# Kernel tuning notes

Measured on AMD Instinct MI355X. Metric: run time of the kernel, lower is better.

## Reference

```python
import jax, jax.numpy as jnp
import numpy as np

TOP_K = 2  # num_experts_per_tok


def setup_inputs() -> dict:
    key = jax.random.key(0)
    k1, k2, k3, k4, k5 = jax.random.split(key, 5)
    B, S, D, F, E = 2, 1024, 1024, 2048, 8
    return {
        "x": jax.random.normal(k1, (B, S, D), dtype=jnp.float32),
        "router_kernel_DE": jax.random.normal(k2, (D, E), dtype=jnp.float32) * 0.02,
        "kernel_gating_EDF": jax.random.normal(k3, (E, D, F), dtype=jnp.float32) * 0.02,
        "kernel_up_EDF": jax.random.normal(k4, (E, D, F), dtype=jnp.float32) * 0.02,
        "kernel_down_EFD": jax.random.normal(k5, (E, F, D), dtype=jnp.float32) * 0.02,
    }


def reference(x, router_kernel_DE, kernel_gating_EDF, kernel_up_EDF, kernel_down_EFD):
    E = router_kernel_DE.shape[-1]
    x = x.astype(jnp.float32)
    # --- Router ---
    logits_BSE = jnp.einsum('BSD,DE->BSE', x, router_kernel_DE)
    probs_BSE = jax.nn.softmax(logits_BSE.astype(jnp.float32), axis=-1)
    weights_BSK, indices_BSK = jax.lax.top_k(probs_BSE, TOP_K)
    norm_weights_BSK = jax.nn.softmax(weights_BSK, axis=-1)
    # scatter top-k weights into dense [B,S,E]
    one_hot_BSKE = jax.nn.one_hot(indices_BSK, num_classes=E, dtype=x.dtype)
    full_weights_BSE = jnp.sum(one_hot_BSKE * norm_weights_BSK[..., None], axis=2)
    # --- Dense-over-all-experts MoE forward ---
    gating_BSEF = jnp.einsum('BSD,EDF->BSEF', x, kernel_gating_EDF)
    act_BSEF = jax.nn.silu(gating_BSEF)
    up_BSEF = jnp.einsum('BSD,EDF->BSEF', x, kernel_up_EDF)
    fuse_BSEF = act_BSEF * up_BSEF
    down_BSED = jnp.einsum('BSEF,EFD->BSED', fuse_BSEF, kernel_down_EFD)
    out_BSD = jnp.einsum('BSED,BSE->BSD', down_BSED, full_weights_BSE)
    return out_BSD.astype(jnp.float32)
```

## Files before the change

kernel.cpp:

```cpp
#include <hip/hip_runtime.h>
#include <hip/hip_bf16.h>
#include <stdint.h>

#define T_TOK 2048
#define DIM 1024
#define FDIM 2048
#define NEXP 8
#define NSLOT 4096
#define MAXTILE 64

typedef short bf16x8 __attribute__((ext_vector_type(8)));
typedef unsigned short u16x8 __attribute__((ext_vector_type(8)));
typedef float f32x4 __attribute__((ext_vector_type(4)));

__device__ __forceinline__ unsigned short f2bf(float f) {
  union { float f; unsigned int u; } v; v.f = f;
  unsigned int r = v.u + 0x7FFFu + ((v.u >> 16) & 1u);
  return (unsigned short)(r >> 16);
}

__device__ __forceinline__ float bf2f(unsigned short x) {
  union { unsigned int u; float f; } v; v.u = ((unsigned int)x) << 16;
  return v.f;
}

__device__ __forceinline__ void gld_lds16(const void* g, void* l) {
  __builtin_amdgcn_global_load_lds(
      (const __attribute__((address_space(1))) unsigned int*)g,
      (__attribute__((address_space(3))) unsigned int*)l, 16, 0, 0);
}

__global__ void router_kernel(const float* __restrict__ x, const float* __restrict__ rk,
                              int* __restrict__ counts, int* __restrict__ tok_e,
                              float* __restrict__ tok_w) {
  int w = threadIdx.x >> 6, lane = threadIdx.x & 63;
  int t = blockIdx.x * 4 + w;
  float acc[NEXP];
#pragma unroll
  for (int e = 0; e < NEXP; ++e) acc[e] = 0.f;
  const float4* xr = (const float4*)(x + (size_t)t * DIM);
#pragma unroll
  for (int i = 0; i < 4; ++i) {
    float4 xv = xr[i * 64 + lane];
    int d0 = (i * 64 + lane) * 4;
#pragma unroll
    for (int j = 0; j < 4; ++j) {
      const float4* rr = (const float4*)(rk + (size_t)(d0 + j) * NEXP);
      float4 r0 = rr[0], r1 = rr[1];
      float xs = (j == 0) ? xv.x : (j == 1) ? xv.y : (j == 2) ? xv.z : xv.w;
      acc[0] += xs * r0.x; acc[1] += xs * r0.y; acc[2] += xs * r0.z; acc[3] += xs * r0.w;
      acc[4] += xs * r1.x; acc[5] += xs * r1.y; acc[6] += xs * r1.z; acc[7] += xs * r1.w;
    }
  }
#pragma unroll
  for (int off = 32; off > 0; off >>= 1) {
#pragma unroll
    for (int e = 0; e < NEXP; ++e) acc[e] += __shfl_xor(acc[e], off, 64);
  }
  if (lane == 0) {
    float m = acc[0];
    for (int e = 1; e < NEXP; ++e) m = fmaxf(m, acc[e]);
    float p[NEXP], s = 0.f;
    for (int e = 0; e < NEXP; ++e) { p[e] = expf(acc[e] - m); s += p[e]; }
    float inv = 1.f / s;
    for (int e = 0; e < NEXP; ++e) p[e] *= inv;
    int i1 = 0;
    for (int e = 1; e < NEXP; ++e) if (p[e] > p[i1]) i1 = e;
    int i2 = (i1 == 0) ? 1 : 0;
    for (int e = 0; e < NEXP; ++e) if (e != i1 && p[e] > p[i2]) i2 = e;
    float e1 = expf(p[i1]), e2 = expf(p[i2]);
    float winv = 1.f / (e1 + e2);
    tok_e[t * 2] = i1; tok_e[t * 2 + 1] = i2;
    tok_w[t * 2] = e1 * winv; tok_w[t * 2 + 1] = e2 * winv;
    atomicAdd(&counts[i1], 1); atomicAdd(&counts[i2], 1);
  }
}

__global__ void scan_kernel(const int* __restrict__ counts, int* __restrict__ offsets,
                            int* __restrict__ tile_e, int* __restrict__ tile_mt,
                            int* __restrict__ ntiles) {
  if (threadIdx.x == 0) {
    int s = 0, t = 0;
    for (int e = 0; e < NEXP; ++e) {
      offsets[e] = s; s += counts[e];
      int nt = (counts[e] + 127) >> 7;
      for (int m = 0; m < nt; ++m) { tile_e[t] = e; tile_mt[t] = m; ++t; }
    }
    ntiles[0] = t;
  }
}

__global__ void assign_kernel(const int* __restrict__ tok_e, const float* __restrict__ tok_w,
                              const int* __restrict__ offsets, int* __restrict__ cursor,
                              int* __restrict__ slot_token, float* __restrict__ slot_weight,
                              int* __restrict__ tok_slot) {
  int t = blockIdx.x * 256 + threadIdx.x;
  if (t >= T_TOK) return;
#pragma unroll
  for (int k = 0; k < 2; ++k) {
    int e = tok_e[t * 2 + k];
    int pos = atomicAdd(&cursor[e], 1);
    int slot = offsets[e] + pos;
    slot_token[slot] = t;
    slot_weight[slot] = tok_w[t * 2 + k];
    tok_slot[t * 2 + k] = slot;
  }
}

__global__ void cvt_x_kernel(const float* __restrict__ x, unsigned short* __restrict__ xb) {
  int i = blockIdx.x * 256 + threadIdx.x;
  const float4* p = (const float4*)x;
  float4 a = p[i * 2], b = p[i * 2 + 1];
  uint4 o;
  o.x = ((unsigned)f2bf(a.y) << 16) | f2bf(a.x);
  o.y = ((unsigned)f2bf(a.w) << 16) | f2bf(a.z);
  o.z = ((unsigned)f2bf(b.y) << 16) | f2bf(b.x);
  o.w = ((unsigned)f2bf(b.w) << 16) | f2bf(b.z);
  ((uint4*)xb)[i] = o;
}

__global__ void transpose_cvt_kernel(const float* __restrict__ in, unsigned short* __restrict__ out,
                                     int R, int C) {
  __shared__ float lds[64][65];
  int e = blockIdx.z;
  size_t base = (size_t)e * (size_t)R * (size_t)C;
  int rb = blockIdx.y * 64, cb = blockIdx.x * 64;
  int tid = threadIdx.x;
  int col4 = (tid & 15) * 4, row = tid >> 4;
#pragma unroll
  for (int it = 0; it < 4; ++it) {
    int r = row + it * 16;
    float4 v = *(const float4*)(in + base + (size_t)(rb + r) * C + cb + col4);
    lds[col4 + 0][r] = v.x; lds[col4 + 1][r] = v.y;
    lds[col4 + 2][r] = v.z; lds[col4 + 3][r] = v.w;
  }
  __syncthreads();
  int r2 = (tid & 31) * 2, c = tid >> 5;
#pragma unroll
  for (int it = 0; it < 8; ++it) {
    int cc = c + it * 8;
    unsigned v = ((unsigned)f2bf(lds[cc][r2 + 1]) << 16) | f2bf(lds[cc][r2]);
    *(unsigned*)(out + base + (size_t)(cb + cc) * R + rb + r2) = v;
  }
}


__global__ __launch_bounds__(256) void gemm_gateup(
    const unsigned short* __restrict__ xb, const unsigned short* __restrict__ wg,
    const unsigned short* __restrict__ wu, const int* __restrict__ counts,
    const int* __restrict__ offsets, const int* __restrict__ slot_token,
    const int* __restrict__ tile_e, const int* __restrict__ tile_mt,
    const int* __restrict__ ntiles, unsigned short* __restrict__ fuse) {
  int ys = blockIdx.y;
  if (ys >= ntiles[0]) return;
  int e = tile_e[ys], mt = tile_mt[ys];
  int cnt = counts[e];
  int off = offsets[e];
  int nt = blockIdx.x;
  __shared__ unsigned short Al[128 * 64];
  __shared__ unsigned short Bgl[64 * 64];
  __shared__ unsigned short Bul[64 * 64];
  int tid = threadIdx.x, w = tid >> 6, lane = tid & 63;
  int csrc = ((lane & 7) ^ (lane >> 3)) * 8;
  unsigned aoff[4];
  unsigned boff[2];
#pragma unroll
  for (int ii = 0; ii < 4; ++ii) {
    int r = (w * 4 + ii) * 8 + (lane >> 3);
    int row = mt * 128 + r;
    int tok = (row < cnt) ? slot_token[off + row] : 0;
    aoff[ii] = (unsigned)(tok * DIM + csrc);
  }
#pragma unroll
  for (int ii = 0; ii < 2; ++ii) {
    int r = (w * 2 + ii) * 8 + (lane >> 3);
    boff[ii] = (unsigned)((e * FDIM + nt * 64 + r) * DIM + csrc);
  }
  f32x4 accg[4][2] = {};
  f32x4 accu[4][2] = {};
  int wr = (w >> 1) * 64, wc = (w & 1) * 32;
  int swz = (lane & 7) << 3;
  int kof0 = ((lane >> 4) * 8) ^ swz;
  int kof1 = (32 + (lane >> 4) * 8) ^ swz;
  for (int k0 = 0; k0 < DIM; k0 += 64) {
#pragma unroll
    for (int ii = 0; ii < 4; ++ii)
      gld_lds16(xb + aoff[ii] + k0, &Al[(w * 4 + ii) * 512]);
#pragma unroll
    for (int ii = 0; ii < 2; ++ii) {
      gld_lds16(wg + boff[ii] + k0, &Bgl[(w * 2 + ii) * 512]);
      gld_lds16(wu + boff[ii] + k0, &Bul[(w * 2 + ii) * 512]);
    }
    __syncthreads();
#pragma unroll
    for (int kk = 0; kk < 2; ++kk) {
      int kof = kk ? kof1 : kof0;
      bf16x8 af[4], bg[2], bu[2];
#pragma unroll
      for (int q = 0; q < 4; ++q)
        af[q] = *(const bf16x8*)&Al[(wr + q * 16 + (lane & 15)) * 64 + kof];
#pragma unroll
      for (int q = 0; q < 2; ++q) {
        bg[q] = *(const bf16x8*)&Bgl[(wc + q * 16 + (lane & 15)) * 64 + kof];
        bu[q] = *(const bf16x8*)&Bul[(wc + q * 16 + (lane & 15)) * 64 + kof];
      }
#pragma unroll
      for (int m4 = 0; m4 < 4; ++m4) {
#pragma unroll
        for (int n4 = 0; n4 < 2; ++n4) {
          accg[m4][n4] = __builtin_amdgcn_mfma_f32_16x16x32_bf16(af[m4], bg[n4], accg[m4][n4], 0, 0, 0);
          accu[m4][n4] = __builtin_amdgcn_mfma_f32_16x16x32_bf16(af[m4], bu[n4], accu[m4][n4], 0, 0, 0);
        }
      }
    }
    __syncthreads();
  }
#pragma unroll
  for (int m4 = 0; m4 < 4; ++m4) {
#pragma unroll
    for (int n4 = 0; n4 < 2; ++n4) {
      f32x4 g = accg[m4][n4], u = accu[m4][n4];
#pragma unroll
      for (int j = 0; j < 4; ++j) {
        int r = wr + m4 * 16 + (lane >> 4) * 4 + j;
        int row = mt * 128 + r;
        if (row < cnt) {
          float gv = g[j];
          float val = gv / (1.f + expf(-gv)) * u[j];
          int f = nt * 64 + wc + n4 * 16 + (lane & 15);
          fuse[(size_t)(off + row) * FDIM + f] = f2bf(val);
        }
      }
    }
  }
}

__global__ __launch_bounds__(256) void gemm_down(
    const unsigned short* __restrict__ fuse, const unsigned short* __restrict__ wd,
    const int* __restrict__ counts, const int* __restrict__ offsets,
    const float* __restrict__ slot_weight, const int* __restrict__ tile_e,
    const int* __restrict__ tile_mt, const int* __restrict__ ntiles,
    unsigned short* __restrict__ part2) {
  int ys = blockIdx.y;
  if (ys >= ntiles[0]) return;
  int e = tile_e[ys], mt = tile_mt[ys];
  int cnt = counts[e];
  int off = offsets[e];
  int nt = blockIdx.x;
  int z = blockIdx.z;
  int kbase = z * (FDIM / 2);
  __shared__ unsigned short Al[128 * 64];
  __shared__ unsigned short Bl[64 * 64];
  int tid = threadIdx.x, w = tid >> 6, lane = tid & 63;
  int csrc = ((lane & 7) ^ (lane >> 3)) * 8;
  unsigned aoff[4];
  unsigned boff[2];
#pragma unroll
  for (int ii = 0; ii < 4; ++ii) {
    int r = (w * 4 + ii) * 8 + (lane >> 3);
    int row = mt * 128 + r;
    int grow = (row < cnt) ? (off + row) : off;
    aoff[ii] = (unsigned)(grow * FDIM + kbase + csrc);
  }
#pragma unroll
  for (int ii = 0; ii < 2; ++ii) {
    int r = (w * 2 + ii) * 8 + (lane >> 3);
    boff[ii] = (unsigned)((e * DIM + nt * 64 + r) * FDIM + kbase + csrc);
  }
  f32x4 acc[4][2] = {};
  int wr = (w >> 1) * 64, wc = (w & 1) * 32;
  int swz = (lane & 7) << 3;
  int kof0 = ((lane >> 4) * 8) ^ swz;
  int kof1 = (32 + (lane >> 4) * 8) ^ swz;
  for (int k0 = 0; k0 < FDIM / 2; k0 += 64) {
#pragma unroll
    for (int ii = 0; ii < 4; ++ii)
      gld_lds16(fuse + aoff[ii] + k0, &Al[(w * 4 + ii) * 512]);
#pragma unroll
    for (int ii = 0; ii < 2; ++ii)
      gld_lds16(wd + boff[ii] + k0, &Bl[(w * 2 + ii) * 512]);
    __syncthreads();
#pragma unroll
    for (int kk = 0; kk < 2; ++kk) {
      int kof = kk ? kof1 : kof0;
      bf16x8 af[4], bfr[2];
#pragma unroll
      for (int q = 0; q < 4; ++q)
        af[q] = *(const bf16x8*)&Al[(wr + q * 16 + (lane & 15)) * 64 + kof];
#pragma unroll
      for (int q = 0; q < 2; ++q)
        bfr[q] = *(const bf16x8*)&Bl[(wc + q * 16 + (lane & 15)) * 64 + kof];
#pragma unroll
      for (int m4 = 0; m4 < 4; ++m4) {
#pragma unroll
        for (int n4 = 0; n4 < 2; ++n4) {
          acc[m4][n4] = __builtin_amdgcn_mfma_f32_16x16x32_bf16(af[m4], bfr[n4], acc[m4][n4], 0, 0, 0);
        }
      }
    }
    __syncthreads();
  }
#pragma unroll
  for (int m4 = 0; m4 < 4; ++m4) {
#pragma unroll
    for (int j = 0; j < 4; ++j) {
      int r = wr + m4 * 16 + (lane >> 4) * 4 + j;
      int row = mt * 128 + r;
      if (row < cnt) {
        float wgt = slot_weight[off + row];
#pragma unroll
        for (int n4 = 0; n4 < 2; ++n4) {
          int d = nt * 64 + wc + n4 * 16 + (lane & 15);
          part2[((size_t)z * NSLOT + off + row) * DIM + d] = f2bf(acc[m4][n4][j] * wgt);
        }
      }
    }
  }
}

__global__ void combine_kernel(const unsigned short* __restrict__ part2,
                               const int* __restrict__ tok_slot, float* __restrict__ out) {
  int i = blockIdx.x * 256 + threadIdx.x;
  int t = i >> 7;
  int c = i & 127;
  int s0 = tok_slot[t * 2], s1 = tok_slot[t * 2 + 1];
  const u16x8* base = (const u16x8*)part2;
  u16x8 a0 = base[((size_t)s0) * (DIM / 8) + c];
  u16x8 a1 = base[((size_t)NSLOT + s0) * (DIM / 8) + c];
  u16x8 b0 = base[((size_t)s1) * (DIM / 8) + c];
  u16x8 b1 = base[((size_t)NSLOT + s1) * (DIM / 8) + c];
  float o[8];
#pragma unroll
  for (int j = 0; j < 8; ++j)
    o[j] = (bf2f(a0[j]) + bf2f(a1[j])) + (bf2f(b0[j]) + bf2f(b1[j]));
  float4* dst = (float4*)(out + (size_t)t * DIM + c * 8);
  dst[0] = make_float4(o[0], o[1], o[2], o[3]);
  dst[1] = make_float4(o[4], o[5], o[6], o[7]);
}

extern "C" void kernel_launch(void* const* d_in, const int* in_sizes, int n_in,
                              void* d_out, int out_size, void* d_ws, size_t ws_size,
                              hipStream_t stream) {
  (void)in_sizes; (void)n_in; (void)out_size;
  const float* x    = (const float*)d_in[0];
  const float* rk   = (const float*)d_in[1];
  const float* wg_f = (const float*)d_in[2];
  const float* wu_f = (const float*)d_in[3];
  const float* wd_f = (const float*)d_in[4];
  float* out = (float*)d_out;

  char* ws = (char*)d_ws;
  size_t o_xb   = 0;
  size_t o_wg   = o_xb + (size_t)T_TOK * DIM * 2;
  size_t o_wu   = o_wg + (size_t)NEXP * FDIM * DIM * 2;
  size_t o_wd   = o_wu + (size_t)NEXP * FDIM * DIM * 2;
  size_t o_fuse = o_wd + (size_t)NEXP * DIM * FDIM * 2;
  size_t o_part = o_fuse + (size_t)NSLOT * FDIM * 2;
  size_t o_meta = o_part + (size_t)2 * NSLOT * DIM * 2;
  size_t o_counts = o_meta;
  size_t o_cursor = o_counts + 32;
  size_t o_offs   = o_cursor + 32;
  size_t o_tok_e  = o_offs + 32;
  size_t o_tok_w  = o_tok_e + (size_t)T_TOK * 2 * 4;
  size_t o_tok_s  = o_tok_w + (size_t)T_TOK * 2 * 4;
  size_t o_st     = o_tok_s + (size_t)T_TOK * 2 * 4;
  size_t o_sw     = o_st + (size_t)NSLOT * 4;
  size_t o_te     = o_sw + (size_t)NSLOT * 4;
  size_t o_tm     = o_te + MAXTILE * 4;
  size_t o_ntl    = o_tm + MAXTILE * 4;
  size_t need     = o_ntl + 32;
  if (ws_size < need) return;

  unsigned short* xb    = (unsigned short*)(ws + o_xb);
  unsigned short* wgt   = (unsigned short*)(ws + o_wg);
  unsigned short* wut   = (unsigned short*)(ws + o_wu);
  unsigned short* wdt   = (unsigned short*)(ws + o_wd);
  unsigned short* fuse  = (unsigned short*)(ws + o_fuse);
  unsigned short* part2 = (unsigned short*)(ws + o_part);
  int* counts          = (int*)(ws + o_counts);
  int* cursor          = (int*)(ws + o_cursor);
  int* offsets         = (int*)(ws + o_offs);
  int* tok_e           = (int*)(ws + o_tok_e);
  float* tok_w         = (float*)(ws + o_tok_w);
  int* tok_slot        = (int*)(ws + o_tok_s);
  int* slot_token      = (int*)(ws + o_st);
  float* slot_weight   = (float*)(ws + o_sw);
  int* tile_e          = (int*)(ws + o_te);
  int* tile_mt         = (int*)(ws + o_tm);
  int* ntiles          = (int*)(ws + o_ntl);

  hipMemsetAsync(ws + o_counts, 0, 64, stream);
  router_kernel<<<T_TOK / 4, 256, 0, stream>>>(x, rk, counts, tok_e, tok_w);
  scan_kernel<<<1, 64, 0, stream>>>(counts, offsets, tile_e, tile_mt, ntiles);
  assign_kernel<<<T_TOK / 256, 256, 0, stream>>>(tok_e, tok_w, offsets, cursor,
                                                 slot_token, slot_weight, tok_slot);
  cvt_x_kernel<<<(T_TOK * DIM / 8) / 256, 256, 0, stream>>>(x, xb);
  transpose_cvt_kernel<<<dim3(FDIM / 64, DIM / 64, NEXP), 256, 0, stream>>>(wg_f, wgt, DIM, FDIM);
  transpose_cvt_kernel<<<dim3(FDIM / 64, DIM / 64, NEXP), 256, 0, stream>>>(wu_f, wut, DIM, FDIM);
  transpose_cvt_kernel<<<dim3(DIM / 64, FDIM / 64, NEXP), 256, 0, stream>>>(wd_f, wdt, FDIM, DIM);

  gemm_gateup<<<dim3(FDIM / 64, 40, 1), 256, 0, stream>>>(
      xb, wgt, wut, counts, offsets, slot_token, tile_e, tile_mt, ntiles, fuse);
  gemm_down<<<dim3(DIM / 64, 40, 2), 256, 0, stream>>>(
      fuse, wdt, counts, offsets, slot_weight, tile_e, tile_mt, ntiles, part2);
  combine_kernel<<<(T_TOK * DIM / 8) / 256, 256, 0, stream>>>(part2, tok_slot, out);
}
```

Measured before the change: 260.2 us.

## Double-buffer LDS tiles with K=32 stages in gate/up and down GEMMs

Both expert GEMM kernels now use two LDS buffers with a 32-wide K slice each. The loads for the next slice are issued before the MFMA compute on the current slice, with explicit waitcnt and barrier sync between stages. The goal is to hide global-to-LDS load latency behind compute, where the old code serialized load, sync and compute. The cost is twice as many barriers per K and a new swizzle layout for the smaller tile.

```diff
diff --git a/kernel.cpp b/kernel.cpp
--- a/kernel.cpp
+++ b/kernel.cpp
@@ -29,6 +29,12 @@
       (const __attribute__((address_space(1))) unsigned int*)g,
       (__attribute__((address_space(3))) unsigned int*)l, 16, 0, 0);
 }
+
+#define PIPE_SYNC()                                        \
+  __builtin_amdgcn_sched_barrier(0);                       \
+  asm volatile("s_waitcnt vmcnt(0)" ::: "memory");         \
+  __builtin_amdgcn_s_barrier();                            \
+  __builtin_amdgcn_sched_barrier(0)
 
 __global__ void router_kernel(const float* __restrict__ x, const float* __restrict__ rk,
                               int* __restrict__ counts, int* __restrict__ tok_e,
@@ -157,64 +163,71 @@
   int cnt = counts[e];
   int off = offsets[e];
   int nt = blockIdx.x;
-  __shared__ unsigned short Al[128 * 64];
-  __shared__ unsigned short Bgl[64 * 64];
-  __shared__ unsigned short Bul[64 * 64];
+  __shared__ unsigned short Al[2][128 * 32];
+  __shared__ unsigned short Bgl[2][64 * 32];
+  __shared__ unsigned short Bul[2][64 * 32];
   int tid = threadIdx.x, w = tid >> 6, lane = tid & 63;
-  int csrc = ((lane & 7) ^ (lane >> 3)) * 8;
-  unsigned aoff[4];
-  unsigned boff[2];
-#pragma unroll
-  for (int ii = 0; ii < 4; ++ii) {
-    int r = (w * 4 + ii) * 8 + (lane >> 3);
+  int csrc = (((lane & 3) ^ ((lane >> 2) & 3))) * 8;
+  unsigned aoff[2];
+  unsigned boff;
+#pragma unroll
+  for (int ii = 0; ii < 2; ++ii) {
+    int j = ii * 4 + w;
+    int r = j * 16 + (lane >> 2);
     int row = mt * 128 + r;
     int tok = (row < cnt) ? slot_token[off + row] : 0;
     aoff[ii] = (unsigned)(tok * DIM + csrc);
   }
-#pragma unroll
-  for (int ii = 0; ii < 2; ++ii) {
-    int r = (w * 2 + ii) * 8 + (lane >> 3);
-    boff[ii] = (unsigned)((e * FDIM + nt * 64 + r) * DIM + csrc);
+  {
+    int r = w * 16 + (lane >> 2);
+    boff = (unsigned)((e * FDIM + nt * 64 + r) * DIM + csrc);
   }
   f32x4 accg[4][2] = {};
   f32x4 accu[4][2] = {};
   int wr = (w >> 1) * 64, wc = (w & 1) * 32;
-  int swz = (lane & 7) << 3;
-  int kof0 = ((lane >> 4) * 8) ^ swz;
-  int kof1 = (32 + (lane >> 4) * 8) ^ swz;
-  for (int k0 = 0; k0 < DIM; k0 += 64) {
-#pragma unroll
-    for (int ii = 0; ii < 4; ++ii)
-      gld_lds16(xb + aoff[ii] + k0, &Al[(w * 4 + ii) * 512]);
-#pragma unroll
-    for (int ii = 0; ii < 2; ++ii) {
-      gld_lds16(wg + boff[ii] + k0, &Bgl[(w * 2 + ii) * 512]);
-      gld_lds16(wu + boff[ii] + k0, &Bul[(w * 2 + ii) * 512]);
-    }
-    __syncthreads();
-#pragma unroll
-    for (int kk = 0; kk < 2; ++kk) {
-      int kof = kk ? kof1 : kof0;
-      bf16x8 af[4], bg[2], bu[2];
-#pragma unroll
-      for (int q = 0; q < 4; ++q)
-        af[q] = *(const bf16x8*)&Al[(wr + q * 16 + (lane & 15)) * 64 + kof];
-#pragma unroll
-      for (int q = 0; q < 2; ++q) {
-        bg[q] = *(const bf16x8*)&Bgl[(wc + q * 16 + (lane & 15)) * 64 + kof];
-        bu[q] = *(const bf16x8*)&Bul[(wc + q * 16 + (lane & 15)) * 64 + kof];
+  int kof = ((lane >> 4) ^ (lane & 3)) * 8;
+
+  auto stage = [&](int buf, int k0) {
+    gld_lds16(xb + aoff[0] + k0, &Al[buf][(0 * 4 + w) * 512]);
+    gld_lds16(xb + aoff[1] + k0, &Al[buf][(1 * 4 + w) * 512]);
+    gld_lds16(wg + boff + k0, &Bgl[buf][w * 512]);
+    gld_lds16(wu + boff + k0, &Bul[buf][w * 512]);
+  };
+  auto compute = [&](int buf) {
+    bf16x8 af[4], bg[2], bu[2];
+#pragma unroll
+    for (int q = 0; q < 4; ++q)
+      af[q] = *(const bf16x8*)&Al[buf][(wr + q * 16 + (lane & 15)) * 32 + kof];
+#pragma unroll
+    for (int q = 0; q < 2; ++q) {
+      bg[q] = *(const bf16x8*)&Bgl[buf][(wc + q * 16 + (lane & 15)) * 32 + kof];
+      bu[q] = *(const bf16x8*)&Bul[buf][(wc + q * 16 + (lane & 15)) * 32 + kof];
+    }
+#pragma unroll
+    for (int m4 = 0; m4 < 4; ++m4) {
+#pragma unroll
+      for (int n4 = 0; n4 < 2; ++n4) {
+        accg[m4][n4] = __builtin_amdgcn_mfma_f32_16x16x32_bf16(af[m4], bg[n4], accg[m4][n4], 0, 0, 0);
+        accu[m4][n4] = __builtin_amdgcn_mfma_f32_16x16x32_bf16(af[m4], bu[n4], accu[m4][n4], 0, 0, 0);
       }
-#pragma unroll
-      for (int m4 = 0; m4 < 4; ++m4) {
-#pragma unroll
-        for (int n4 = 0; n4 < 2; ++n4) {
-          accg[m4][n4] = __builtin_amdgcn_mfma_f32_16x16x32_bf16(af[m4], bg[n4], accg[m4][n4], 0, 0, 0);
-          accu[m4][n4] = __builtin_amdgcn_mfma_f32_16x16x32_bf16(af[m4], bu[n4], accu[m4][n4], 0, 0, 0);
-        }
-      }
-    }
-    __syncthreads();
-  }
+    }
+  };
+
+  stage(0, 0);
+  PIPE_SYNC();
+  for (int t = 0; t < 30; t += 2) {
+    stage(1, (t + 1) * 32);
+    compute(0);
+    PIPE_SYNC();
+    stage(0, (t + 2) * 32);
+    compute(1);
+    PIPE_SYNC();
+  }
+  stage(1, 31 * 32);
+  compute(0);
+  PIPE_SYNC();
+  compute(1);
+
 #pragma unroll
   for (int m4 = 0; m4 < 4; ++m4) {
 #pragma unroll
@@ -249,57 +262,65 @@
   int nt = blockIdx.x;
   int z = blockIdx.z;
   int kbase = z * (FDIM / 2);
-  __shared__ unsigned short Al[128 * 64];
-  __shared__ unsigned short Bl[64 * 64];
+  __shared__ unsigned short Al[2][128 * 32];
+  __shared__ unsigned short Bl[2][64 * 32];
   int tid = threadIdx.x, w = tid >> 6, lane = tid & 63;
-  int csrc = ((lane & 7) ^ (lane >> 3)) * 8;
-  unsigned aoff[4];
-  unsigned boff[2];
-#pragma unroll
-  for (int ii = 0; ii < 4; ++ii) {
-    int r = (w * 4 + ii) * 8 + (lane >> 3);
+  int csrc = (((lane & 3) ^ ((lane >> 2) & 3))) * 8;
+  unsigned aoff[2];
+  unsigned boff;
+#pragma unroll
+  for (int ii = 0; ii < 2; ++ii) {
+    int j = ii * 4 + w;
+    int r = j * 16 + (lane >> 2);
     int row = mt * 128 + r;
     int grow = (row < cnt) ? (off + row) : off;
     aoff[ii] = (unsigned)(grow * FDIM + kbase + csrc);
   }
-#pragma unroll
-  for (int ii = 0; ii < 2; ++ii) {
-    int r = (w * 2 + ii) * 8 + (lane >> 3);
-    boff[ii] = (unsigned)((e * DIM + nt * 64 + r) * FDIM + kbase + csrc);
+  {
+    int r = w * 16 + (lane >> 2);
+    boff = (unsigned)((e * DIM + nt * 64 + r) * FDIM + kbase + csrc);
   }
   f32x4 acc[4][2] = {};
   int wr = (w >> 1) * 64, wc = (w & 1) * 32;
-  int swz = (lane & 7) << 3;
-  int kof0 = ((lane >> 4) * 8) ^ swz;
-  int kof1 = (32 + (lane >> 4) * 8) ^ swz;
-  for (int k0 = 0; k0 < FDIM / 2; k0 += 64) {
-#pragma unroll
-    for (int ii = 0; ii < 4; ++ii)
-      gld_lds16(fuse + aoff[ii] + k0, &Al[(w * 4 + ii) * 512]);
-#pragma unroll
-    for (int ii = 0; ii < 2; ++ii)
-      gld_lds16(wd + boff[ii] + k0, &Bl[(w * 2 + ii) * 512]);
-    __syncthreads();
-#pragma unroll
-    for (int kk = 0; kk < 2; ++kk) {
-      int kof = kk ? kof1 : kof0;
-      bf16x8 af[4], bfr[2];
-#pragma unroll
-      for (int q = 0; q < 4; ++q)
-        af[q] = *(const bf16x8*)&Al[(wr + q * 16 + (lane & 15)) * 64 + kof];
-#pragma unroll
-      for (int q = 0; q < 2; ++q)
-        bfr[q] = *(const bf16x8*)&Bl[(wc + q * 16 + (lane & 15)) * 64 + kof];
-#pragma unroll
-      for (int m4 = 0; m4 < 4; ++m4) {
-#pragma unroll
-        for (int n4 = 0; n4 < 2; ++n4) {
-          acc[m4][n4] = __builtin_amdgcn_mfma_f32_16x16x32_bf16(af[m4], bfr[n4], acc[m4][n4], 0, 0, 0);
-        }
+  int kof = ((lane >> 4) ^ (lane & 3)) * 8;
+
+  auto stage = [&](int buf, int k0) {
+    gld_lds16(fuse + aoff[0] + k0, &Al[buf][(0 * 4 + w) * 512]);
+    gld_lds16(fuse + aoff[1] + k0, &Al[buf][(1 * 4 + w) * 512]);
+    gld_lds16(wd + boff + k0, &Bl[buf][w * 512]);
+  };
+  auto compute = [&](int buf) {
+    bf16x8 af[4], bfr[2];
+#pragma unroll
+    for (int q = 0; q < 4; ++q)
+      af[q] = *(const bf16x8*)&Al[buf][(wr + q * 16 + (lane & 15)) * 32 + kof];
+#pragma unroll
+    for (int q = 0; q < 2; ++q)
+      bfr[q] = *(const bf16x8*)&Bl[buf][(wc + q * 16 + (lane & 15)) * 32 + kof];
+#pragma unroll
+    for (int m4 = 0; m4 < 4; ++m4) {
+#pragma unroll
+      for (int n4 = 0; n4 < 2; ++n4) {
+        acc[m4][n4] = __builtin_amdgcn_mfma_f32_16x16x32_bf16(af[m4], bfr[n4], acc[m4][n4], 0, 0, 0);
       }
     }
-    __syncthreads();
-  }
+  };
+
+  stage(0, 0);
+  PIPE_SYNC();
+  for (int t = 0; t < 30; t += 2) {
+    stage(1, (t + 1) * 32);
+    compute(0);
+    PIPE_SYNC();
+    stage(0, (t + 2) * 32);
+    compute(1);
+    PIPE_SYNC();
+  }
+  stage(1, 31 * 32);
+  compute(0);
+  PIPE_SYNC();
+  compute(1);
+
 #pragma unroll
   for (int m4 = 0; m4 < 4; ++m4) {
 #pragma unroll
```

New measurement: 291.7 us. 1.12x slower.
